# Performance work log

Hardware: AMD Instinct MI355X
Metric: run time of the kernel (lower is better)

## Reference

```python
import jax, jax.numpy as jnp
import numpy as np

# Module config (matches init_kwargs)
H, W = 1024, 1024
PATCH = 128
OVERLAP = 2
STRIDE = PATCH - OVERLAP                      # 126
H_PAD = H + PATCH - H % STRIDE                # 1136
W_PAD = W + PATCH - W % STRIDE                # 1136
NH = H_PAD // STRIDE                          # 9
NW = W_PAD // STRIDE                          # 9
C = 64


def setup_inputs() -> dict:
    key = jax.random.key(0)
    x = jax.random.normal(key, (NH * NW, C, PATCH, PATCH), dtype=jnp.float32)
    return {"x": x}


def reference(x) -> jnp.ndarray:
    # Original: row-major loop over (i, j) overwrites overlapping patches into a
    # stride < patch, every output pixel (y, w) is last written by patch
    # (i, j) = (y // stride, w // stride) (clipped to the grid), at local
    # offset (y - i*stride, w - j*stride). Express this as a single fused
    # gather instead of N slice-assignment kernels.
    ys = jnp.arange(H)
    ws = jnp.arange(W)
    iy = jnp.minimum(ys // STRIDE, NH - 1)          # [H] patch row index
    jx = jnp.minimum(ws // STRIDE, NW - 1)          # [W] patch col index
    offy = ys - iy * STRIDE                         # [H] row offset inside patch
    offx = ws - jx * STRIDE                         # [W] col offset inside patch
    patch_idx = iy[:, None] * NW + jx[None, :]      # [H, W] flat patch index
    # Advanced indexing (advanced idx split by the channel slice) -> [H, W, C]
    out_hwc = x[patch_idx, :, offy[:, None], offx[None, :]]
    return jnp.transpose(out_hwc, (2, 0, 1))        # [C, H, W]
```

## Files before the change

kernel.cpp:

```cpp
#include <hip/hip_runtime.h>


__global__ __launch_bounds__(256) void patch_gather_kernel(
    const float* __restrict__ x, float* __restrict__ out, unsigned n_groups) {
    const unsigned stride = gridDim.x * blockDim.x;
    for (unsigned g = blockIdx.x * blockDim.x + threadIdx.x; g < n_groups; g += stride) {
        const unsigned idx = g << 2;
        const unsigned c  = idx >> 20;
        const unsigned y  = (idx >> 10) & 1023u;
        const unsigned w0 = idx & 1023u;

        const unsigned iy = y / 126u;
        const unsigned oy = y - iy * 126u;

        float v[4];
        #pragma unroll
        for (int k = 0; k < 4; ++k) {
            const unsigned w  = w0 + k;
            const unsigned jx = w / 126u;
            const unsigned ox = w - jx * 126u;
            const unsigned p  = iy * 9u + jx;
            const size_t addr = ((size_t)(p * 64u + c) << 14) + (oy << 7) + ox;
            v[k] = x[addr];
        }
        float4 r;
        r.x = v[0]; r.y = v[1]; r.z = v[2]; r.w = v[3];
        *reinterpret_cast<float4*>(&out[idx]) = r;
    }
}

extern "C" void kernel_launch(void* const* d_in, const int* in_sizes, int n_in,
                              void* d_out, int out_size, void* d_ws, size_t ws_size,
                              hipStream_t stream) {
    const float* x = (const float*)d_in[0];
    float* out = (float*)d_out;

    const unsigned n_groups = (unsigned)(out_size / 4);
    const int block = 256;
    unsigned total_blocks = (n_groups + block - 1) / block;
    unsigned grid = total_blocks < 2048u ? total_blocks : 2048u;

    patch_gather_kernel<<<grid, block, 0, stream>>>(x, out, n_groups);
}
```

Baseline: 118.2 us.

## Stage patch rows in LDS with aligned float4 loads before gathering output rows

Each block now handles 32 output rows in groups of 8. For each row it loads the 1040 contiguous patch floats (8 patches wide, 130 columns each) from global memory into shared memory with aligned float4 loads, then assembles output rows from LDS using float2 reads. This replaces per-element scalar global gathers with vectorized coalesced loads. In exchange it reads some extra overlap columns, adds LDS traffic and barriers, and hardcodes the grid size to 2048 blocks.

After: 146.9 us. 1.24x slower.

```diff
diff --git a/kernel.cpp b/kernel.cpp
--- a/kernel.cpp
+++ b/kernel.cpp
@@ -1,31 +1,52 @@
 #include <hip/hip_runtime.h>
 
 
-__global__ __launch_bounds__(256) void patch_gather_kernel(
-    const float* __restrict__ x, float* __restrict__ out, unsigned n_groups) {
-    const unsigned stride = gridDim.x * blockDim.x;
-    for (unsigned g = blockIdx.x * blockDim.x + threadIdx.x; g < n_groups; g += stride) {
-        const unsigned idx = g << 2;
-        const unsigned c  = idx >> 20;
-        const unsigned y  = (idx >> 10) & 1023u;
-        const unsigned w0 = idx & 1023u;
+__global__ __launch_bounds__(256) void patch_gather_lds(
+    const float* __restrict__ x, float* __restrict__ out) {
+    __shared__ float lds[8][1040];
+    const unsigned t = threadIdx.x;
+    const unsigned Rblock = blockIdx.x * 32u;
 
-        const unsigned iy = y / 126u;
-        const unsigned oy = y - iy * 126u;
+    for (unsigned g = 0; g < 4u; ++g) {
+        const unsigned R0 = Rblock + g * 8u;
 
-        float v[4];
         #pragma unroll
-        for (int k = 0; k < 4; ++k) {
-            const unsigned w  = w0 + k;
-            const unsigned jx = w / 126u;
-            const unsigned ox = w - jx * 126u;
-            const unsigned p  = iy * 9u + jx;
-            const size_t addr = ((size_t)(p * 64u + c) << 14) + (oy << 7) + ox;
-            v[k] = x[addr];
+        for (unsigned p = 0; p < 9u; ++p) {
+            const unsigned q = t + p * 256u;
+            if (q < 2080u) {
+                const unsigned r  = q / 260u;
+                const unsigned u  = q - r * 260u;
+                const unsigned R  = R0 + r;
+                const unsigned c  = R >> 10;
+                const unsigned y  = R & 1023u;
+                const unsigned iy = y / 126u;
+                const unsigned oy = y - iy * 126u;
+                const unsigned jx = u >> 5;
+                const size_t addr = ((size_t)((iy * 9u + jx) * 64u + c) << 14)
+                                  + (oy << 7) + ((u & 31u) << 2);
+                *reinterpret_cast<float4*>(&lds[0][0] + 4u * q) =
+                    *reinterpret_cast<const float4*>(&x[addr]);
+            }
         }
-        float4 r;
-        r.x = v[0]; r.y = v[1]; r.z = v[2]; r.w = v[3];
-        *reinterpret_cast<float4*>(&out[idx]) = r;
+        __syncthreads();
+
+        const unsigned w0  = t << 2;
+        const unsigned jxA = w0 / 126u;
+        const unsigned oxA = w0 - jxA * 126u;
+        const unsigned w2  = w0 + 2u;
+        const unsigned jxB = w2 / 126u;
+        const unsigned oxB = w2 - jxB * 126u;
+        const unsigned offA = (jxA << 7) + oxA;
+        const unsigned offB = (jxB << 7) + oxB;
+        #pragma unroll
+        for (unsigned p = 0; p < 8u; ++p) {
+            const float2 a = *reinterpret_cast<const float2*>(&lds[p][offA]);
+            const float2 b = *reinterpret_cast<const float2*>(&lds[p][offB]);
+            float4 v; v.x = a.x; v.y = a.y; v.z = b.x; v.w = b.y;
+            const unsigned R = R0 + p;
+            *reinterpret_cast<float4*>(&out[((size_t)R << 10) + w0]) = v;
+        }
+        __syncthreads();
     }
 }
 
@@ -34,11 +55,5 @@
                               hipStream_t stream) {
     const float* x = (const float*)d_in[0];
     float* out = (float*)d_out;
-
-    const unsigned n_groups = (unsigned)(out_size / 4);
-    const int block = 256;
-    unsigned total_blocks = (n_groups + block - 1) / block;
-    unsigned grid = total_blocks < 2048u ? total_blocks : 2048u;
-
-    patch_gather_kernel<<<grid, block, 0, stream>>>(x, out, n_groups);
+    patch_gather_lds<<<2048, 256, 0, stream>>>(x, out);
 }
```
